# Kernel optimization log

Measured on AMD Instinct MI355X. Metric: run time of the kernel, lower is better.

## Reference

```python
import jax, jax.numpy as jnp
import numpy as np
import math

D_MODEL = 2048
N_HEADS = 16
HEAD_DIM = 128
ROPE_THETA = 10000.0


def apply_rope(x, pos, theta=ROPE_THETA):
    # x: [b, h, s, d], pos: [b, s] int
    d = x.shape[-1]
    inv_freq = 1.0 / (theta ** (jnp.arange(0, d, 2, dtype=jnp.float32) / d))  # [d/2]
    ang = pos.astype(jnp.float32)[:, None, :, None] * inv_freq  # [b,1,s,d/2]
    cos, sin = jnp.cos(ang), jnp.sin(ang)
    x1, x2 = x[..., 0::2], x[..., 1::2]
    out_even = x1 * cos - x2 * sin
    out_odd = x1 * sin + x2 * cos
    return jnp.stack([out_even, out_odd], axis=-1).reshape(x.shape)


def setup_inputs() -> dict:
    key = jax.random.key(0)
    ks = jax.random.split(key, 5)
    b, s = 2, 2048
    scale = 1.0 / math.sqrt(D_MODEL)
    x = jax.random.normal(ks[0], (b, s, D_MODEL), dtype=jnp.float32)
    Wq = jax.random.normal(ks[1], (D_MODEL, D_MODEL), dtype=jnp.float32) * scale
    Wk = jax.random.normal(ks[2], (D_MODEL, D_MODEL), dtype=jnp.float32) * scale
    Wv = jax.random.normal(ks[3], (D_MODEL, D_MODEL), dtype=jnp.float32) * scale
    Wo = jax.random.normal(ks[4], (D_MODEL, D_MODEL), dtype=jnp.float32) * scale
    token_positions = jnp.broadcast_to(jnp.arange(s, dtype=jnp.int32), (b, s))
    return {"x": x, "token_positions": token_positions, "Wq": Wq, "Wk": Wk, "Wv": Wv, "Wo": Wo}


def reference(x, token_positions, Wq, Wk, Wv, Wo):
    b, s, _ = x.shape
    h, d = N_HEADS, HEAD_DIM
    # QKV projections (Linear: x @ W.T), split heads: b s (h d) -> b h s d
    def proj(W):
        y = jnp.einsum('bse,fe->bsf', x, W)
        return y.reshape(b, s, h, d).transpose(0, 2, 1, 3)
    Q, K, V = proj(Wq), proj(Wk), proj(Wv)
    Q = apply_rope(Q, token_positions)
    K = apply_rope(K, token_positions)
    logits = jnp.einsum('bhqd,bhkd->bhqk', Q, K) / math.sqrt(d)
    causal = jnp.triu(jnp.ones((s, s), dtype=bool), 1)
    logits = jnp.where(causal, -jnp.inf, logits)
    attn = jax.nn.softmax(logits, axis=-1)
    ctx = jnp.einsum('bhqk,bhkd->bhqd', attn, V)
    ctx = ctx.transpose(0, 2, 1, 3).reshape(b, s, h * d)
    return jnp.einsum('bsf,ef->bse', ctx, Wo)
```

## Files before the change

kernel.cpp:

```cpp
#include <hip/hip_runtime.h>
#include <cstdint>
#include <cstddef>

typedef __bf16 bf16_t;
typedef __bf16 bf16x8 __attribute__((ext_vector_type(8)));
typedef float  f32x4  __attribute__((ext_vector_type(4)));

#define SEQ 2048
#define NH  16
#define HD  128
#define MM  4096
#define KK  2048

#define ASYNC16(g, l) __builtin_amdgcn_global_load_lds( \
    (const __attribute__((address_space(1))) void*)(g), \
    (__attribute__((address_space(3))) void*)(l), 16, 0, 0)

#define MFMA16(a, b, c) __builtin_amdgcn_mfma_f32_16x16x32_bf16((a), (b), (c), 0, 0, 0)

__global__ __launch_bounds__(256) void cast_all(const float* __restrict__ x,
                                                const float* __restrict__ Wq,
                                                const float* __restrict__ Wk,
                                                const float* __restrict__ Wv,
                                                const float* __restrict__ Wo,
                                                bf16_t* __restrict__ xb,
                                                bf16_t* __restrict__ wqkv,
                                                bf16_t* __restrict__ wob) {
    int i = blockIdx.x * 256 + threadIdx.x;
    const float* src;
    bf16_t* dst;
    int off;
    if (i < 2097152) { src = x; dst = xb; off = i; }
    else {
        int j = i - 2097152;
        int sel = j >> 20; off = j & 0xFFFFF;
        if (sel < 3) { src = (sel == 0) ? Wq : (sel == 1) ? Wk : Wv; dst = wqkv + (size_t)sel * 4194304; }
        else         { src = Wo; dst = wob; }
    }
    float4 v = ((const float4*)src)[off];
    union { bf16_t h[4]; uint2 u; } t;
    t.h[0] = (bf16_t)v.x; t.h[1] = (bf16_t)v.y;
    t.h[2] = (bf16_t)v.z; t.h[3] = (bf16_t)v.w;
    ((uint2*)dst)[off] = t.u;
}

union SMemQ8 {
    bf16_t st[2][32768];
    bf16_t epi[64 * 264];
};

__global__ __launch_bounds__(512, 2) void gemm_qkv(const bf16_t* __restrict__ A,
                                                   const bf16_t* __restrict__ B,
                                                   bf16_t* __restrict__ Qout,
                                                   bf16_t* __restrict__ Kout,
                                                   bf16_t* __restrict__ Vout,
                                                   const int* __restrict__ pos) {
    __shared__ SMemQ8 sm;
    const int tid = threadIdx.x;
    const int w = tid >> 6, l = tid & 63;
    const int lane16 = l & 15, quad = l >> 4;
    const int tm = blockIdx.y, tn = blockIdx.x;
    const int wm = w >> 2, wn = w & 3;

    const int miA0 = wm * 8 + wn;
    const int miA1 = miA0 + 4;
    const int niB0 = (w >> 1) * 4 + (w & 1);
    const int niB1 = niB0 + 2;

    const bf16_t* gA0 = A + (size_t)(tm * 256 + miA0 * 16 + lane16) * KK + quad * 8;
    const bf16_t* gA1 = A + (size_t)(tm * 256 + miA1 * 16 + lane16) * KK + quad * 8;
    const bf16_t* gB0 = B + (size_t)(tn * 256 + niB0 * 16 + lane16) * KK + quad * 8;
    const bf16_t* gB1 = B + (size_t)(tn * 256 + niB1 * 16 + lane16) * KK + quad * 8;

    const int dA0 = miA0 * 1024;
    const int dA1 = miA1 * 1024;
    const int dB0 = 16384 + niB0 * 1024;
    const int dB1 = 16384 + niB1 * 1024;

    f32x4 acc[8][4];
    #pragma unroll
    for (int i = 0; i < 8; i++)
        #pragma unroll
        for (int j = 0; j < 4; j++) acc[i][j] = (f32x4){0.f, 0.f, 0.f, 0.f};

    ASYNC16(gA0,      &sm.st[0][dA0]);
    ASYNC16(gA0 + 32, &sm.st[0][dA0 + 512]);
    ASYNC16(gB0,      &sm.st[0][dB0]);
    ASYNC16(gB0 + 32, &sm.st[0][dB0 + 512]);
    ASYNC16(gB1,      &sm.st[0][dB1]);
    ASYNC16(gB1 + 32, &sm.st[0][dB1 + 512]);
    ASYNC16(gA1,      &sm.st[0][dA1]);
    ASYNC16(gA1 + 32, &sm.st[0][dA1 + 512]);
    gA0 += 64; gA1 += 64; gB0 += 64; gB1 += 64;

    const int NT = KK / 64;
    for (int t = 0; t < NT; ++t) {
        const int buf = t & 1, nbuf = buf ^ 1;
        const bool pf = (t + 1 < NT);
        const bf16_t* sa = &sm.st[buf][0];
        const bf16_t* sb = &sm.st[buf][16384];
        bf16_t* nb = &sm.st[nbuf][0];

        asm volatile("s_waitcnt vmcnt(4) lgkmcnt(0)" ::: "memory");
        __builtin_amdgcn_s_barrier();
        asm volatile("" ::: "memory");
        if (pf) { ASYNC16(gA0, nb + dA0); ASYNC16(gA0 + 32, nb + dA0 + 512); }
        bf16x8 a0[4][2], b0[2][2];
        #pragma unroll
        for (int i = 0; i < 4; i++)
            #pragma unroll
            for (int ks = 0; ks < 2; ks++)
                a0[i][ks] = *(const bf16x8*)(sa + ((wm * 8 + i) * 2 + ks) * 512 + l * 8);
        #pragma unroll
        for (int j = 0; j < 2; j++)
            #pragma unroll
            for (int ks = 0; ks < 2; ks++)
                b0[j][ks] = *(const bf16x8*)(sb + ((wn * 4 + j) * 2 + ks) * 512 + l * 8);
        __builtin_amdgcn_s_setprio(1);
        #pragma unroll
        for (int i = 0; i < 4; i++)
            #pragma unroll
            for (int j = 0; j < 2; j++) {
                acc[i][j] = MFMA16(a0[i][0], b0[j][0], acc[i][j]);
                acc[i][j] = MFMA16(a0[i][1], b0[j][1], acc[i][j]);
            }
        __builtin_amdgcn_s_setprio(0);

        if (pf) { asm volatile("s_waitcnt vmcnt(4)" ::: "memory"); }
        else    { asm volatile("s_waitcnt vmcnt(2)" ::: "memory"); }
        __builtin_amdgcn_s_barrier();
        asm volatile("" ::: "memory");
        if (pf) { ASYNC16(gB0, nb + dB0); ASYNC16(gB0 + 32, nb + dB0 + 512); }
        bf16x8 b1[2][2];
        #pragma unroll
        for (int j = 0; j < 2; j++)
            #pragma unroll
            for (int ks = 0; ks < 2; ks++)
                b1[j][ks] = *(const bf16x8*)(sb + ((wn * 4 + 2 + j) * 2 + ks) * 512 + l * 8);
        __builtin_amdgcn_s_setprio(1);
        #pragma unroll
        for (int i = 0; i < 4; i++)
            #pragma unroll
            for (int j = 0; j < 2; j++) {
                acc[i][2 + j] = MFMA16(a0[i][0], b1[j][0], acc[i][2 + j]);
                acc[i][2 + j] = MFMA16(a0[i][1], b1[j][1], acc[i][2 + j]);
            }
        __builtin_amdgcn_s_setprio(0);

        if (pf) { asm volatile("s_waitcnt vmcnt(4)" ::: "memory"); }
        else    { asm volatile("s_waitcnt vmcnt(0)" ::: "memory"); }
        __builtin_amdgcn_s_barrier();
        asm volatile("" ::: "memory");
        if (pf) { ASYNC16(gB1, nb + dB1); ASYNC16(gB1 + 32, nb + dB1 + 512); }
        bf16x8 a1[4][2];
        #pragma unroll
        for (int i = 0; i < 4; i++)
            #pragma unroll
            for (int ks = 0; ks < 2; ks++)
                a1[i][ks] = *(const bf16x8*)(sa + ((wm * 8 + 4 + i) * 2 + ks) * 512 + l * 8);
        __builtin_amdgcn_s_setprio(1);
        #pragma unroll
        for (int i = 0; i < 4; i++)
            #pragma unroll
            for (int j = 0; j < 2; j++) {
                acc[4 + i][j] = MFMA16(a1[i][0], b0[j][0], acc[4 + i][j]);
                acc[4 + i][j] = MFMA16(a1[i][1], b0[j][1], acc[4 + i][j]);
            }
        __builtin_amdgcn_s_setprio(0);

        if (pf) {
            ASYNC16(gA1, nb + dA1); ASYNC16(gA1 + 32, nb + dA1 + 512);
            gA0 += 64; gA1 += 64; gB0 += 64; gB1 += 64;
        }
        __builtin_amdgcn_s_setprio(1);
        #pragma unroll
        for (int i = 0; i < 4; i++)
            #pragma unroll
            for (int j = 0; j < 2; j++) {
                acc[4 + i][2 + j] = MFMA16(a1[i][0], b1[j][0], acc[4 + i][2 + j]);
                acc[4 + i][2 + j] = MFMA16(a1[i][1], b1[j][1], acc[4 + i][2 + j]);
            }
        __builtin_amdgcn_s_setprio(0);
    }

    const int mbase = tm * 256;
    const int nb2   = tn * 256;
    const int sel   = nb2 >> 11;
    const int hh0   = (nb2 & 2047) >> 7;
    const int bidx  = mbase >> 11;
    const int g   = tid >> 5;
    const int c8  = (tid & 31) * 8;

    if (sel < 2) {
        bf16_t* base = ((sel == 0) ? Qout : Kout) + (size_t)(bidx * NH) * SEQ * HD;
        const float qs = (sel == 0) ? 0.08838834764831845f : 1.0f;
        for (int slice = 0; slice < 4; slice++) {
            __syncthreads();
            if (wm == (slice >> 1)) {
                for (int i2 = 0; i2 < 4; i2++) {
                    const int i = (slice & 1) * 4 + i2;
                    for (int j = 0; j < 4; j++)
                        for (int r = 0; r < 4; r++)
                            sm.epi[(i2 * 16 + quad * 4 + r) * 264 + wn * 64 + j * 16 + lane16] =
                                (bf16_t)acc[i][j][r];
                }
            }
            __syncthreads();
            const int head = hh0 + (c8 >> 7);
            const int d0   = c8 & 127;
            for (int p = 0; p < 4; p++) {
                const int rid = p * 16 + g;
                const int s = (mbase & 2047) + slice * 64 + rid;
                bf16x8 v = *(const bf16x8*)&sm.epi[rid * 264 + c8];
                const float pp = (float)pos[bidx * SEQ + s];
                union { bf16_t h8[8]; uint4 u; } o;
                for (int t = 0; t < 4; t++) {
                    const int fi = (d0 >> 1) + t;
                    const float freq = exp2f(-(float)fi * 0.20762050593045857f);
                    const float ang = pp * freq;
                    const float sn = __sinf(ang), cs = __cosf(ang);
                    const float x1 = (float)v[2 * t], x2 = (float)v[2 * t + 1];
                    o.h8[2 * t]     = (bf16_t)((x1 * cs - x2 * sn) * qs);
                    o.h8[2 * t + 1] = (bf16_t)((x1 * sn + x2 * cs) * qs);
                }
                *(uint4*)(base + (size_t)(head * SEQ + s) * HD + d0) = o.u;
            }
        }
    } else {
        const int s0 = mbase & 2047;
        for (int half = 0; half < 4; half++) {
            __syncthreads();
            if (wn == half) {
                for (int i = 0; i < 8; i++)
                    for (int j = 0; j < 4; j++) {
                        union { bf16_t h4[4]; uint2 u; } pk;
                        for (int r = 0; r < 4; r++) pk.h4[r] = (bf16_t)acc[i][j][r];
                        *(uint2*)&sm.epi[(j * 16 + lane16) * 264 + wm * 128 + i * 16 + quad * 4] = pk.u;
                    }
            }
            __syncthreads();
            const int head = hh0 + (half >> 1);
            bf16_t* dstb = Vout + (size_t)(bidx * NH + head) * HD * SEQ;
            for (int p = 0; p < 4; p++) {
                const int rid = p * 16 + g;
                const int dh  = (half & 1) * 64 + rid;
                bf16x8 v = *(const bf16x8*)&sm.epi[rid * 264 + c8];
                *(uint4*)(dstb + (size_t)dh * SEQ + s0 + c8) = *(const uint4*)&v;
            }
        }
    }
}

union SMemU {
    struct { bf16_t A[3][4096]; bf16_t B[3][4096]; } st;
    bf16_t epi[64 * 136];
};

__global__ __launch_bounds__(256) void gemm_out(const bf16_t* __restrict__ A,
                                                const bf16_t* __restrict__ B,
                                                float* __restrict__ Cout) {
    __shared__ SMemU sm;
    const int tid = threadIdx.x;
    const int w = tid >> 6, l = tid & 63;
    const int lane16 = l & 15, quad = l >> 4;
    const int tm = blockIdx.y, tn = blockIdx.x;
    const int wm = w >> 1, wn = w & 1;

    const bf16_t* pA0 = A + (size_t)(tm * 128 + (2 * w + 0) * 16 + lane16) * KK + quad * 8;
    const bf16_t* pA1 = A + (size_t)(tm * 128 + (2 * w + 1) * 16 + lane16) * KK + quad * 8;
    const bf16_t* pB0 = B + (size_t)(tn * 128 + (2 * w + 0) * 16 + lane16) * KK + quad * 8;
    const bf16_t* pB1 = B + (size_t)(tn * 128 + (2 * w + 1) * 16 + lane16) * KK + quad * 8;

    f32x4 acc[4][4];
    for (int i = 0; i < 4; i++)
        for (int j = 0; j < 4; j++) acc[i][j] = (f32x4){0.f, 0.f, 0.f, 0.f};

    ASYNC16(pA0,      &sm.st.A[0][(2 * w + 0) * 512]);
    ASYNC16(pA1,      &sm.st.A[0][(2 * w + 1) * 512]);
    ASYNC16(pB0,      &sm.st.B[0][(2 * w + 0) * 512]);
    ASYNC16(pB1,      &sm.st.B[0][(2 * w + 1) * 512]);
    ASYNC16(pA0 + 32, &sm.st.A[1][(2 * w + 0) * 512]);
    ASYNC16(pA1 + 32, &sm.st.A[1][(2 * w + 1) * 512]);
    ASYNC16(pB0 + 32, &sm.st.B[1][(2 * w + 0) * 512]);
    ASYNC16(pB1 + 32, &sm.st.B[1][(2 * w + 1) * 512]);

    const bf16_t* qA0 = pA0 + 64;
    const bf16_t* qA1 = pA1 + 64;
    const bf16_t* qB0 = pB0 + 64;
    const bf16_t* qB1 = pB1 + 64;

    const int NT = KK / 32;
    int rdbuf = 0, stbuf = 2;
    for (int t = 0; t < NT; ++t) {
        if (t == NT - 1) { asm volatile("s_waitcnt vmcnt(0) lgkmcnt(0)" ::: "memory"); }
        else             { asm volatile("s_waitcnt vmcnt(4) lgkmcnt(0)" ::: "memory"); }
        __builtin_amdgcn_s_barrier();
        asm volatile("" ::: "memory");
        if (t + 2 < NT) {
            ASYNC16(qA0, &sm.st.A[stbuf][(2 * w + 0) * 512]);
            ASYNC16(qA1, &sm.st.A[stbuf][(2 * w + 1) * 512]);
            ASYNC16(qB0, &sm.st.B[stbuf][(2 * w + 0) * 512]);
            ASYNC16(qB1, &sm.st.B[stbuf][(2 * w + 1) * 512]);
            qA0 += 32; qA1 += 32; qB0 += 32; qB1 += 32;
            stbuf = (stbuf == 2) ? 0 : stbuf + 1;
        }
        const bf16_t* rA = &sm.st.A[rdbuf][wm * 2048 + l * 8];
        const bf16_t* rB = &sm.st.B[rdbuf][wn * 2048 + l * 8];
        bf16x8 af[4], bfr[4];
        for (int i = 0; i < 4; i++) af[i]  = *(const bf16x8*)(rA + i * 512);
        for (int j = 0; j < 4; j++) bfr[j] = *(const bf16x8*)(rB + j * 512);
        for (int i = 0; i < 4; i++)
            for (int j = 0; j < 4; j++)
                acc[i][j] = MFMA16(af[i], bfr[j], acc[i][j]);
        rdbuf = (rdbuf == 2) ? 0 : rdbuf + 1;
    }

    const int mbase = tm * 128 + wm * 64;
    const int nbase = tn * 128 + wn * 64;
    for (int i = 0; i < 4; i++)
        for (int j = 0; j < 4; j++) {
            const int n  = nbase + j * 16 + lane16;
            const int m0 = mbase + i * 16 + quad * 4;
            for (int r = 0; r < 4; r++)
                Cout[(size_t)(m0 + r) * 2048 + n] = acc[i][j][r];
        }
}

__global__ __launch_bounds__(256) void attn_kernel(const bf16_t* __restrict__ Q,
                                                   const bf16_t* __restrict__ K,
                                                   const bf16_t* __restrict__ Vt,
                                                   bf16_t* __restrict__ ctx) {
    const int flat = blockIdx.x;
    const int bh = flat & 31;
    const int bt = flat >> 5;
    const int h = bh & 15, b = bh >> 4;
    const bf16_t* Qh = Q  + (size_t)bh * SEQ * HD;
    const bf16_t* Kh = K  + (size_t)bh * SEQ * HD;
    const bf16_t* Vh = Vt + (size_t)bh * HD * SEQ;

    const int tid = threadIdx.x;
    const int w = tid >> 6, l = tid & 63;
    const int lane16 = l & 15, quad = l >> 4;

    __shared__ bf16_t kt[2][16 * 512];
    __shared__ bf16_t vt[2][16 * 512];
    __shared__ bf16_t pbuf[4][1024];

    for (int half = 0; half < 2; half++) {
        const int qt = half ? (31 - bt) : bt;
        const int q0 = qt * 64 + w * 16;

        bf16x8 qf[4];
        {
            const bf16_t* qrow = Qh + (size_t)(q0 + lane16) * HD + quad * 8;
            for (int kc = 0; kc < 4; kc++) qf[kc] = *(const bf16x8*)(qrow + kc * 32);
        }

        f32x4 o[8];
        for (int dt = 0; dt < 8; dt++) o[dt] = (f32x4){0.f, 0.f, 0.f, 0.f};
        float m_s = -INFINITY, l_s = 0.f;

        __syncthreads();
        for (int ii = 0; ii < 4; ii++) {
            const int f = w * 4 + ii;
            const int nt = f >> 2, kc = f & 3;
            ASYNC16(Kh + (size_t)(nt * 16 + lane16) * HD + kc * 32 + quad * 8, &kt[0][f * 512]);
            const int dt = f >> 1, kk = f & 1;
            ASYNC16(Vh + (size_t)(dt * 16 + lane16) * SEQ + kk * 32 + quad * 8, &vt[0][f * 512]);
        }

        int cur = 0;
        for (int kb = 0; kb <= qt; kb++) {
            const int k0 = kb * 64;
            __syncthreads();
            if (kb < qt) {
                const int kn = k0 + 64;
                for (int ii = 0; ii < 4; ii++) {
                    const int f = w * 4 + ii;
                    const int nt = f >> 2, kc = f & 3;
                    ASYNC16(Kh + (size_t)(kn + nt * 16 + lane16) * HD + kc * 32 + quad * 8,
                            &kt[1 - cur][f * 512]);
                    const int dt = f >> 1, kk = f & 1;
                    ASYNC16(Vh + (size_t)(dt * 16 + lane16) * SEQ + kn + kk * 32 + quad * 8,
                            &vt[1 - cur][f * 512]);
                }
            }
            const bf16_t* ktc = kt[cur];
            const bf16_t* vtc = vt[cur];

            f32x4 sacc[4];
            for (int nt = 0; nt < 4; nt++) sacc[nt] = (f32x4){0.f, 0.f, 0.f, 0.f};
            __builtin_amdgcn_s_setprio(1);
            for (int nt = 0; nt < 4; nt++)
                for (int kc = 0; kc < 4; kc++) {
                    bf16x8 kf = *(const bf16x8*)&ktc[(nt * 4 + kc) * 512 + l * 8];
                    sacc[nt] = MFMA16(kf, qf[kc], sacc[nt]);
                }
            __builtin_amdgcn_s_setprio(0);
            if (kb == qt) {
                const int qg = q0 + lane16;
                for (int nt = 0; nt < 4; nt++)
                    for (int r = 0; r < 4; r++) {
                        const int kg = k0 + nt * 16 + quad * 4 + r;
                        if (kg > qg) sacc[nt][r] = -INFINITY;
                    }
            }
            float rmnt[4];
            for (int nt = 0; nt < 4; nt++)
                rmnt[nt] = fmaxf(fmaxf(sacc[nt][0], sacc[nt][1]),
                                 fmaxf(sacc[nt][2], sacc[nt][3]));
            float rowmax = fmaxf(fmaxf(rmnt[0], rmnt[1]), fmaxf(rmnt[2], rmnt[3]));
            rowmax = fmaxf(rowmax, __shfl_xor(rowmax, 16, 64));
            rowmax = fmaxf(rowmax, __shfl_xor(rowmax, 32, 64));

            float a = 1.f;
            const bool noresc = __all(rowmax <= m_s + 8.f) != 0;
            if (!noresc) {
                const float mnew = fmaxf(m_s, rowmax);
                a = __expf(m_s - mnew);
                m_s = mnew;
            }
            float ssum = 0.f;
            for (int nt = 0; nt < 4; nt++) {
                union { bf16_t h4[4]; uint2 u; } pk;
                for (int r = 0; r < 4; r++) {
                    const float e = __expf(sacc[nt][r] - m_s);
                    ssum += e;
                    pk.h4[r] = (bf16_t)e;
                }
                const int addr = (nt >> 1) * 512 +
                                 (((nt & 1) * 2 + (quad >> 1)) * 16 + lane16) * 8 +
                                 (quad & 1) * 4;
                *(uint2*)&pbuf[w][addr] = pk.u;
            }
            ssum += __shfl_xor(ssum, 16, 64);
            ssum += __shfl_xor(ssum, 32, 64);
            l_s = l_s * a + ssum;

            if (!noresc) {
                float ar[4];
                for (int r = 0; r < 4; r++) ar[r] = __shfl(a, (quad << 2) | r, 16);
                for (int dt = 0; dt < 8; dt++)
                    for (int r = 0; r < 4; r++) o[dt][r] *= ar[r];
            }
            __builtin_amdgcn_s_setprio(1);
            for (int kk = 0; kk < 2; kk++) {
                bf16x8 pf = *(const bf16x8*)&pbuf[w][kk * 512 + l * 8];
                for (int dt = 0; dt < 8; dt++) {
                    bf16x8 vf = *(const bf16x8*)&vtc[(dt * 2 + kk) * 512 + l * 8];
                    o[dt] = MFMA16(pf, vf, o[dt]);
                }
            }
            __builtin_amdgcn_s_setprio(0);
            cur ^= 1;
        }

        float inv[4];
        for (int r = 0; r < 4; r++) inv[r] = 1.0f / __shfl(l_s, (quad << 2) | r, 16);
        for (int r = 0; r < 4; r++) {
            const int qg = q0 + quad * 4 + r;
            bf16_t* dst = ctx + ((size_t)(b * SEQ + qg)) * (NH * HD) + h * HD;
            for (int dt = 0; dt < 8; dt++)
                dst[dt * 16 + lane16] = (bf16_t)(o[dt][r] * inv[r]);
        }
        __syncthreads();
    }
}

extern "C" void kernel_launch(void* const* d_in, const int* in_sizes, int n_in,
                              void* d_out, int out_size, void* d_ws, size_t ws_size,
                              hipStream_t stream) {
    const float* x  = (const float*)d_in[0];
    const int* pos  = (const int*)d_in[1];
    const float* Wq = (const float*)d_in[2];
    const float* Wk = (const float*)d_in[3];
    const float* Wv = (const float*)d_in[4];
    const float* Wo = (const float*)d_in[5];

    char* ws = (char*)d_ws;
    bf16_t* xb   = (bf16_t*)(ws);
    bf16_t* wqkv = (bf16_t*)(ws + (16u << 20));
    bf16_t* wob  = (bf16_t*)(ws + (40u << 20));
    bf16_t* Qb   = (bf16_t*)(ws + (48u << 20));
    bf16_t* Kb   = (bf16_t*)(ws + (64u << 20));
    bf16_t* Vt   = (bf16_t*)(ws + (80u << 20));
    bf16_t* ctx  = (bf16_t*)(ws + (96u << 20));

    cast_all<<<24576, 256, 0, stream>>>(x, Wq, Wk, Wv, Wo, xb, wqkv, wob);

    dim3 gq(6144 / 256, MM / 256);
    gemm_qkv<<<gq, 512, 0, stream>>>(xb, wqkv, Qb, Kb, Vt, pos);

    attn_kernel<<<512, 256, 0, stream>>>(Qb, Kb, Vt, ctx);

    dim3 gg(2048 / 128, MM / 128);
    gemm_out<<<gg, 256, 0, stream>>>(ctx, wob, (float*)d_out);
}
```

Before: 414.1 us.

## Process paired query tiles together sharing K/V loads; switch softmax to exp2

The attention kernel now handles both of its query tiles (bt and 31-bt) in a single pass over the key blocks. Each K/V tile loaded into LDS is reused for both tiles, and the second sequential loop with its reloads of the shared prefix is gone. The Q scale now folds in log2(e) so softmax can use exp2f, and the rescale threshold is adjusted to match. The kernel also sets launch_bounds to 2 blocks per SM; holding two sets of accumulators raises register pressure and may cause spills.

```diff
diff --git a/kernel.cpp b/kernel.cpp
--- a/kernel.cpp
+++ b/kernel.cpp
@@ -193,7 +193,7 @@
 
     if (sel < 2) {
         bf16_t* base = ((sel == 0) ? Qout : Kout) + (size_t)(bidx * NH) * SEQ * HD;
-        const float qs = (sel == 0) ? 0.08838834764831845f : 1.0f;
+        const float qs = (sel == 0) ? 0.12751742770560996f : 1.0f;
         for (int slice = 0; slice < 4; slice++) {
             __syncthreads();
             if (wm == (slice >> 1)) {
@@ -326,10 +326,60 @@
         }
 }
 
-__global__ __launch_bounds__(256) void attn_kernel(const bf16_t* __restrict__ Q,
-                                                   const bf16_t* __restrict__ K,
-                                                   const bf16_t* __restrict__ Vt,
-                                                   bf16_t* __restrict__ ctx) {
+__device__ __forceinline__ void sm_pv(f32x4* sacc, float& m_s, float& l_s, f32x4* o,
+                                      bf16_t* pbw, const bf16_t* vtc,
+                                      int lane16, int quad, int l) {
+    float rmnt[4];
+    for (int nt = 0; nt < 4; nt++)
+        rmnt[nt] = fmaxf(fmaxf(sacc[nt][0], sacc[nt][1]),
+                         fmaxf(sacc[nt][2], sacc[nt][3]));
+    float rowmax = fmaxf(fmaxf(rmnt[0], rmnt[1]), fmaxf(rmnt[2], rmnt[3]));
+    rowmax = fmaxf(rowmax, __shfl_xor(rowmax, 16, 64));
+    rowmax = fmaxf(rowmax, __shfl_xor(rowmax, 32, 64));
+    float a = 1.f;
+    const bool noresc = __all(rowmax <= m_s + 11.5f) != 0;
+    if (!noresc) {
+        const float mnew = fmaxf(m_s, rowmax);
+        a = exp2f(m_s - mnew);
+        m_s = mnew;
+    }
+    float ssum = 0.f;
+    for (int nt = 0; nt < 4; nt++) {
+        union { bf16_t h4[4]; uint2 u; } pk;
+        for (int r = 0; r < 4; r++) {
+            const float e = exp2f(sacc[nt][r] - m_s);
+            ssum += e;
+            pk.h4[r] = (bf16_t)e;
+        }
+        const int addr = (nt >> 1) * 512 +
+                         (((nt & 1) * 2 + (quad >> 1)) * 16 + lane16) * 8 +
+                         (quad & 1) * 4;
+        *(uint2*)&pbw[addr] = pk.u;
+    }
+    ssum += __shfl_xor(ssum, 16, 64);
+    ssum += __shfl_xor(ssum, 32, 64);
+    l_s = l_s * a + ssum;
+    if (!noresc) {
+        float ar[4];
+        for (int r = 0; r < 4; r++) ar[r] = __shfl(a, (quad << 2) | r, 16);
+        for (int dt = 0; dt < 8; dt++)
+            for (int r = 0; r < 4; r++) o[dt][r] *= ar[r];
+    }
+    __builtin_amdgcn_s_setprio(1);
+    for (int kk = 0; kk < 2; kk++) {
+        bf16x8 pf = *(const bf16x8*)&pbw[kk * 512 + l * 8];
+        for (int dt = 0; dt < 8; dt++) {
+            bf16x8 vf = *(const bf16x8*)&vtc[(dt * 2 + kk) * 512 + l * 8];
+            o[dt] = MFMA16(pf, vf, o[dt]);
+        }
+    }
+    __builtin_amdgcn_s_setprio(0);
+}
+
+__global__ __launch_bounds__(256, 2) void attn_kernel(const bf16_t* __restrict__ Q,
+                                                      const bf16_t* __restrict__ K,
+                                                      const bf16_t* __restrict__ Vt,
+                                                      bf16_t* __restrict__ ctx) {
     const int flat = blockIdx.x;
     const int bh = flat & 31;
     const int bt = flat >> 5;
@@ -346,124 +396,119 @@
     __shared__ bf16_t vt[2][16 * 512];
     __shared__ bf16_t pbuf[4][1024];
 
-    for (int half = 0; half < 2; half++) {
-        const int qt = half ? (31 - bt) : bt;
-        const int q0 = qt * 64 + w * 16;
-
-        bf16x8 qf[4];
+    const int qtA = bt;
+    const int qtB = 31 - bt;
+    const int q0A = qtA * 64 + w * 16;
+    const int q0B = qtB * 64 + w * 16;
+
+    bf16x8 qfA[4], qfB[4];
+    {
+        const bf16_t* qra = Qh + (size_t)(q0A + lane16) * HD + quad * 8;
+        const bf16_t* qrb = Qh + (size_t)(q0B + lane16) * HD + quad * 8;
+        for (int kc = 0; kc < 4; kc++) {
+            qfA[kc] = *(const bf16x8*)(qra + kc * 32);
+            qfB[kc] = *(const bf16x8*)(qrb + kc * 32);
+        }
+    }
+
+    f32x4 oA[8], oB[8];
+    for (int dt = 0; dt < 8; dt++) {
+        oA[dt] = (f32x4){0.f, 0.f, 0.f, 0.f};
+        oB[dt] = (f32x4){0.f, 0.f, 0.f, 0.f};
+    }
+    float mA = -INFINITY, lA = 0.f;
+    float mB = -INFINITY, lB = 0.f;
+
+    for (int ii = 0; ii < 4; ii++) {
+        const int f = w * 4 + ii;
+        const int nt = f >> 2, kc = f & 3;
+        ASYNC16(Kh + (size_t)(nt * 16 + lane16) * HD + kc * 32 + quad * 8, &kt[0][f * 512]);
+        const int dt = f >> 1, kk = f & 1;
+        ASYNC16(Vh + (size_t)(dt * 16 + lane16) * SEQ + kk * 32 + quad * 8, &vt[0][f * 512]);
+    }
+
+    int cur = 0;
+    for (int kb = 0; kb <= qtB; kb++) {
+        const int k0 = kb * 64;
+        __syncthreads();
+        if (kb < qtB) {
+            const int kn = k0 + 64;
+            for (int ii = 0; ii < 4; ii++) {
+                const int f = w * 4 + ii;
+                const int nt = f >> 2, kc = f & 3;
+                ASYNC16(Kh + (size_t)(kn + nt * 16 + lane16) * HD + kc * 32 + quad * 8,
+                        &kt[1 - cur][f * 512]);
+                const int dt = f >> 1, kk = f & 1;
+                ASYNC16(Vh + (size_t)(dt * 16 + lane16) * SEQ + kn + kk * 32 + quad * 8,
+                        &vt[1 - cur][f * 512]);
+            }
+        }
+        const bf16_t* ktc = kt[cur];
+        const bf16_t* vtc = vt[cur];
+
         {
-            const bf16_t* qrow = Qh + (size_t)(q0 + lane16) * HD + quad * 8;
-            for (int kc = 0; kc < 4; kc++) qf[kc] = *(const bf16x8*)(qrow + kc * 32);
-        }
-
-        f32x4 o[8];
-        for (int dt = 0; dt < 8; dt++) o[dt] = (f32x4){0.f, 0.f, 0.f, 0.f};
-        float m_s = -INFINITY, l_s = 0.f;
-
-        __syncthreads();
-        for (int ii = 0; ii < 4; ii++) {
-            const int f = w * 4 + ii;
-            const int nt = f >> 2, kc = f & 3;
-            ASYNC16(Kh + (size_t)(nt * 16 + lane16) * HD + kc * 32 + quad * 8, &kt[0][f * 512]);
-            const int dt = f >> 1, kk = f & 1;
-            ASYNC16(Vh + (size_t)(dt * 16 + lane16) * SEQ + kk * 32 + quad * 8, &vt[0][f * 512]);
-        }
-
-        int cur = 0;
-        for (int kb = 0; kb <= qt; kb++) {
-            const int k0 = kb * 64;
-            __syncthreads();
-            if (kb < qt) {
-                const int kn = k0 + 64;
-                for (int ii = 0; ii < 4; ii++) {
-                    const int f = w * 4 + ii;
-                    const int nt = f >> 2, kc = f & 3;
-                    ASYNC16(Kh + (size_t)(kn + nt * 16 + lane16) * HD + kc * 32 + quad * 8,
-                            &kt[1 - cur][f * 512]);
-                    const int dt = f >> 1, kk = f & 1;
-                    ASYNC16(Vh + (size_t)(dt * 16 + lane16) * SEQ + kn + kk * 32 + quad * 8,
-                            &vt[1 - cur][f * 512]);
-                }
-            }
-            const bf16_t* ktc = kt[cur];
-            const bf16_t* vtc = vt[cur];
-
             f32x4 sacc[4];
             for (int nt = 0; nt < 4; nt++) sacc[nt] = (f32x4){0.f, 0.f, 0.f, 0.f};
             __builtin_amdgcn_s_setprio(1);
             for (int nt = 0; nt < 4; nt++)
                 for (int kc = 0; kc < 4; kc++) {
                     bf16x8 kf = *(const bf16x8*)&ktc[(nt * 4 + kc) * 512 + l * 8];
-                    sacc[nt] = MFMA16(kf, qf[kc], sacc[nt]);
+                    sacc[nt] = MFMA16(kf, qfB[kc], sacc[nt]);
                 }
             __builtin_amdgcn_s_setprio(0);
-            if (kb == qt) {
-                const int qg = q0 + lane16;
+            if (kb == qtB) {
+                const int qg = q0B + lane16;
                 for (int nt = 0; nt < 4; nt++)
                     for (int r = 0; r < 4; r++) {
                         const int kg = k0 + nt * 16 + quad * 4 + r;
                         if (kg > qg) sacc[nt][r] = -INFINITY;
                     }
             }
-            float rmnt[4];
+            sm_pv(sacc, mB, lB, oB, pbuf[w], vtc, lane16, quad, l);
+        }
+
+        if (kb <= qtA) {
+            f32x4 sacc[4];
+            for (int nt = 0; nt < 4; nt++) sacc[nt] = (f32x4){0.f, 0.f, 0.f, 0.f};
+            __builtin_amdgcn_s_setprio(1);
             for (int nt = 0; nt < 4; nt++)
-                rmnt[nt] = fmaxf(fmaxf(sacc[nt][0], sacc[nt][1]),
-                                 fmaxf(sacc[nt][2], sacc[nt][3]));
-            float rowmax = fmaxf(fmaxf(rmnt[0], rmnt[1]), fmaxf(rmnt[2], rmnt[3]));
-            rowmax = fmaxf(rowmax, __shfl_xor(rowmax, 16, 64));
-            rowmax = fmaxf(rowmax, __shfl_xor(rowmax, 32, 64));
-
-            float a = 1.f;
-            const bool noresc = __all(rowmax <= m_s + 8.f) != 0;
-            if (!noresc) {
-                const float mnew = fmaxf(m_s, rowmax);
-                a = __expf(m_s - mnew);
-                m_s = mnew;
-            }
-            float ssum = 0.f;
-            for (int nt = 0; nt < 4; nt++) {
-                union { bf16_t h4[4]; uint2 u; } pk;
-                for (int r = 0; r < 4; r++) {
-                    const float e = __expf(sacc[nt][r] - m_s);
-                    ssum += e;
-                    pk.h4[r] = (bf16_t)e;
+                for (int kc = 0; kc < 4; kc++) {
+                    bf16x8 kf = *(const bf16x8*)&ktc[(nt * 4 + kc) * 512 + l * 8];
+                    sacc[nt] = MFMA16(kf, qfA[kc], sacc[nt]);
                 }
-                const int addr = (nt >> 1) * 512 +
-                                 (((nt & 1) * 2 + (quad >> 1)) * 16 + lane16) * 8 +
-                                 (quad & 1) * 4;
-                *(uint2*)&pbuf[w][addr] = pk.u;
-            }
-            ssum += __shfl_xor(ssum, 16, 64);
-            ssum += __shfl_xor(ssum, 32, 64);
-            l_s = l_s * a + ssum;
-
-            if (!noresc) {
-                float ar[4];
-                for (int r = 0; r < 4; r++) ar[r] = __shfl(a, (quad << 2) | r, 16);
-                for (int dt = 0; dt < 8; dt++)
-                    for (int r = 0; r < 4; r++) o[dt][r] *= ar[r];
-            }
-            __builtin_amdgcn_s_setprio(1);
-            for (int kk = 0; kk < 2; kk++) {
-                bf16x8 pf = *(const bf16x8*)&pbuf[w][kk * 512 + l * 8];
-                for (int dt = 0; dt < 8; dt++) {
-                    bf16x8 vf = *(const bf16x8*)&vtc[(dt * 2 + kk) * 512 + l * 8];
-                    o[dt] = MFMA16(pf, vf, o[dt]);
-                }
-            }
             __builtin_amdgcn_s_setprio(0);
-            cur ^= 1;
-        }
-
+            if (kb == qtA) {
+                const int qg = q0A + lane16;
+                for (int nt = 0; nt < 4; nt++)
+                    for (int r = 0; r < 4; r++) {
+                        const int kg = k0 + nt * 16 + quad * 4 + r;
+                        if (kg > qg) sacc[nt][r] = -INFINITY;
+                    }
+            }
+            sm_pv(sacc, mA, lA, oA, pbuf[w], vtc, lane16, quad, l);
+        }
+        cur ^= 1;
+    }
+
+    {
         float inv[4];
-        for (int r = 0; r < 4; r++) inv[r] = 1.0f / __shfl(l_s, (quad << 2) | r, 16);
+        for (int r = 0; r < 4; r++) inv[r] = 1.0f / __shfl(lA, (quad << 2) | r, 16);
         for (int r = 0; r < 4; r++) {
-            const int qg = q0 + quad * 4 + r;
+            const int qg = q0A + quad * 4 + r;
             bf16_t* dst = ctx + ((size_t)(b * SEQ + qg)) * (NH * HD) + h * HD;
             for (int dt = 0; dt < 8; dt++)
-                dst[dt * 16 + lane16] = (bf16_t)(o[dt][r] * inv[r]);
-        }
-        __syncthreads();
+                dst[dt * 16 + lane16] = (bf16_t)(oA[dt][r] * inv[r]);
+        }
+    }
+    {
+        float inv[4];
+        for (int r = 0; r < 4; r++) inv[r] = 1.0f / __shfl(lB, (quad << 2) | r, 16);
+        for (int r = 0; r < 4; r++) {
+            const int qg = q0B + quad * 4 + r;
+            bf16_t* dst = ctx + ((size_t)(b * SEQ + qg)) * (NH * HD) + h * HD;
+            for (int dt = 0; dt < 8; dt++)
+                dst[dt * 16 + lane16] = (bf16_t)(oB[dt][r] * inv[r]);
+        }
     }
 }
 
```

New measurement: 428.3 us. 1.03x slower.

## Enlarge output GEMM tile to 256x128 with 8 waves and interleaved prefetch

Applied to the files above, without the earlier changes.

The output projection GEMM now uses 512-thread blocks covering a 256x128 tile, so the B tile is reused across twice as many rows and the grid is halved. A single shared staging buffer holds 24 fragments per stage, with each wave loading three, and the waitcnt is adjusted to match. Prefetch loads are interleaved between MFMA groups, and s_setprio raises wave priority around the MFMA bursts. This cuts global traffic for the weight operand at the cost of higher LDS use per block and fewer blocks in flight.

```diff
diff --git a/kernel.cpp b/kernel.cpp
--- a/kernel.cpp
+++ b/kernel.cpp
@@ -251,71 +251,98 @@
     }
 }
 
-union SMemU {
-    struct { bf16_t A[3][4096]; bf16_t B[3][4096]; } st;
-    bf16_t epi[64 * 136];
+union SMemG {
+    bf16_t st[3][24 * 512];
 };
 
-__global__ __launch_bounds__(256) void gemm_out(const bf16_t* __restrict__ A,
-                                                const bf16_t* __restrict__ B,
-                                                float* __restrict__ Cout) {
-    __shared__ SMemU sm;
+__global__ __launch_bounds__(512, 4) void gemm_out(const bf16_t* __restrict__ A,
+                                                   const bf16_t* __restrict__ B,
+                                                   float* __restrict__ Cout) {
+    __shared__ SMemG sm;
     const int tid = threadIdx.x;
     const int w = tid >> 6, l = tid & 63;
     const int lane16 = l & 15, quad = l >> 4;
     const int tm = blockIdx.y, tn = blockIdx.x;
     const int wm = w >> 1, wn = w & 1;
 
-    const bf16_t* pA0 = A + (size_t)(tm * 128 + (2 * w + 0) * 16 + lane16) * KK + quad * 8;
-    const bf16_t* pA1 = A + (size_t)(tm * 128 + (2 * w + 1) * 16 + lane16) * KK + quad * 8;
-    const bf16_t* pB0 = B + (size_t)(tn * 128 + (2 * w + 0) * 16 + lane16) * KK + quad * 8;
-    const bf16_t* pB1 = B + (size_t)(tn * 128 + (2 * w + 1) * 16 + lane16) * KK + quad * 8;
+    const int f0 = 3 * w, f1 = 3 * w + 1, f2 = 3 * w + 2;
+    const bf16_t* p0 = (f0 < 16)
+        ? A + (size_t)(tm * 256 + f0 * 16 + lane16) * KK + quad * 8
+        : B + (size_t)(tn * 128 + (f0 - 16) * 16 + lane16) * KK + quad * 8;
+    const bf16_t* p1 = (f1 < 16)
+        ? A + (size_t)(tm * 256 + f1 * 16 + lane16) * KK + quad * 8
+        : B + (size_t)(tn * 128 + (f1 - 16) * 16 + lane16) * KK + quad * 8;
+    const bf16_t* p2 = (f2 < 16)
+        ? A + (size_t)(tm * 256 + f2 * 16 + lane16) * KK + quad * 8
+        : B + (size_t)(tn * 128 + (f2 - 16) * 16 + lane16) * KK + quad * 8;
 
     f32x4 acc[4][4];
     for (int i = 0; i < 4; i++)
         for (int j = 0; j < 4; j++) acc[i][j] = (f32x4){0.f, 0.f, 0.f, 0.f};
 
-    ASYNC16(pA0,      &sm.st.A[0][(2 * w + 0) * 512]);
-    ASYNC16(pA1,      &sm.st.A[0][(2 * w + 1) * 512]);
-    ASYNC16(pB0,      &sm.st.B[0][(2 * w + 0) * 512]);
-    ASYNC16(pB1,      &sm.st.B[0][(2 * w + 1) * 512]);
-    ASYNC16(pA0 + 32, &sm.st.A[1][(2 * w + 0) * 512]);
-    ASYNC16(pA1 + 32, &sm.st.A[1][(2 * w + 1) * 512]);
-    ASYNC16(pB0 + 32, &sm.st.B[1][(2 * w + 0) * 512]);
-    ASYNC16(pB1 + 32, &sm.st.B[1][(2 * w + 1) * 512]);
-
-    const bf16_t* qA0 = pA0 + 64;
-    const bf16_t* qA1 = pA1 + 64;
-    const bf16_t* qB0 = pB0 + 64;
-    const bf16_t* qB1 = pB1 + 64;
+    ASYNC16(p0,      &sm.st[0][f0 * 512]);
+    ASYNC16(p1,      &sm.st[0][f1 * 512]);
+    ASYNC16(p2,      &sm.st[0][f2 * 512]);
+    ASYNC16(p0 + 32, &sm.st[1][f0 * 512]);
+    ASYNC16(p1 + 32, &sm.st[1][f1 * 512]);
+    ASYNC16(p2 + 32, &sm.st[1][f2 * 512]);
+    p0 += 64; p1 += 64; p2 += 64;
 
     const int NT = KK / 32;
     int rdbuf = 0, stbuf = 2;
     for (int t = 0; t < NT; ++t) {
         if (t == NT - 1) { asm volatile("s_waitcnt vmcnt(0) lgkmcnt(0)" ::: "memory"); }
-        else             { asm volatile("s_waitcnt vmcnt(4) lgkmcnt(0)" ::: "memory"); }
+        else             { asm volatile("s_waitcnt vmcnt(3) lgkmcnt(0)" ::: "memory"); }
         __builtin_amdgcn_s_barrier();
         asm volatile("" ::: "memory");
-        if (t + 2 < NT) {
-            ASYNC16(qA0, &sm.st.A[stbuf][(2 * w + 0) * 512]);
-            ASYNC16(qA1, &sm.st.A[stbuf][(2 * w + 1) * 512]);
-            ASYNC16(qB0, &sm.st.B[stbuf][(2 * w + 0) * 512]);
-            ASYNC16(qB1, &sm.st.B[stbuf][(2 * w + 1) * 512]);
-            qA0 += 32; qA1 += 32; qB0 += 32; qB1 += 32;
-            stbuf = (stbuf == 2) ? 0 : stbuf + 1;
-        }
-        const bf16_t* rA = &sm.st.A[rdbuf][wm * 2048 + l * 8];
-        const bf16_t* rB = &sm.st.B[rdbuf][wn * 2048 + l * 8];
-        bf16x8 af[4], bfr[4];
-        for (int i = 0; i < 4; i++) af[i]  = *(const bf16x8*)(rA + i * 512);
-        for (int j = 0; j < 4; j++) bfr[j] = *(const bf16x8*)(rB + j * 512);
-        for (int i = 0; i < 4; i++)
-            for (int j = 0; j < 4; j++)
-                acc[i][j] = MFMA16(af[i], bfr[j], acc[i][j]);
+
+        const bf16_t* rA = &sm.st[rdbuf][(wm * 4 + 0) * 512 + l * 8];
+        const bf16_t* rB = &sm.st[rdbuf][(16 + wn * 4) * 512 + l * 8];
+        const bool pf = (t + 2 < NT);
+        bf16_t* sb = &sm.st[stbuf][0];
+
+        bf16x8 af0 = *(const bf16x8*)(rA + 0 * 512);
+        bf16x8 af1 = *(const bf16x8*)(rA + 1 * 512);
+        bf16x8 bf0 = *(const bf16x8*)(rB + 0 * 512);
+        bf16x8 bf1 = *(const bf16x8*)(rB + 1 * 512);
+        if (pf) ASYNC16(p0, sb + f0 * 512);
+        __builtin_amdgcn_s_setprio(1);
+        acc[0][0] = MFMA16(af0, bf0, acc[0][0]);
+        acc[0][1] = MFMA16(af0, bf1, acc[0][1]);
+        acc[1][0] = MFMA16(af1, bf0, acc[1][0]);
+        acc[1][1] = MFMA16(af1, bf1, acc[1][1]);
+        __builtin_amdgcn_s_setprio(0);
+
+        bf16x8 af2 = *(const bf16x8*)(rA + 2 * 512);
+        bf16x8 af3 = *(const bf16x8*)(rA + 3 * 512);
+        if (pf) ASYNC16(p1, sb + f1 * 512);
+        __builtin_amdgcn_s_setprio(1);
+        acc[2][0] = MFMA16(af2, bf0, acc[2][0]);
+        acc[2][1] = MFMA16(af2, bf1, acc[2][1]);
+        acc[3][0] = MFMA16(af3, bf0, acc[3][0]);
+        acc[3][1] = MFMA16(af3, bf1, acc[3][1]);
+        __builtin_amdgcn_s_setprio(0);
+
+        bf16x8 bf2 = *(const bf16x8*)(rB + 2 * 512);
+        bf16x8 bf3 = *(const bf16x8*)(rB + 3 * 512);
+        if (pf) ASYNC16(p2, sb + f2 * 512);
+        __builtin_amdgcn_s_setprio(1);
+        acc[0][2] = MFMA16(af0, bf2, acc[0][2]);
+        acc[0][3] = MFMA16(af0, bf3, acc[0][3]);
+        acc[1][2] = MFMA16(af1, bf2, acc[1][2]);
+        acc[1][3] = MFMA16(af1, bf3, acc[1][3]);
+        acc[2][2] = MFMA16(af2, bf2, acc[2][2]);
+        acc[2][3] = MFMA16(af2, bf3, acc[2][3]);
+        acc[3][2] = MFMA16(af3, bf2, acc[3][2]);
+        acc[3][3] = MFMA16(af3, bf3, acc[3][3]);
+        __builtin_amdgcn_s_setprio(0);
+
+        if (pf) { p0 += 32; p1 += 32; p2 += 32; }
         rdbuf = (rdbuf == 2) ? 0 : rdbuf + 1;
+        stbuf = (stbuf == 2) ? 0 : stbuf + 1;
     }
 
-    const int mbase = tm * 128 + wm * 64;
+    const int mbase = tm * 256 + wm * 64;
     const int nbase = tn * 128 + wn * 64;
     for (int i = 0; i < 4; i++)
         for (int j = 0; j < 4; j++) {
@@ -493,6 +520,6 @@
 
     attn_kernel<<<512, 256, 0, stream>>>(Qb, Kb, Vt, ctx);
 
-    dim3 gg(2048 / 128, MM / 128);
-    gemm_out<<<gg, 256, 0, stream>>>(ctx, wob, (float*)d_out);
+    dim3 gg(2048 / 128, MM / 256);
+    gemm_out<<<gg, 512, 0, stream>>>(ctx, wob, (float*)d_out);
 }
```

New measurement: 399.4 us. -3.6%, faster.
